# Optimization experiments

Hardware: AMD Instinct MI355X
Metric: run time of the kernel (lower is better)

Reference implementation:

```python
import jax, jax.numpy as jnp
import numpy as np

N_STATE = 1024
N_HEAD = 16
B, T, S_CACHE = 4, 1024, 3072


def setup_inputs() -> dict:
    key = jax.random.key(0)
    ks = jax.random.split(key, 10)
    d = N_STATE
    inp = {
        "x": jax.random.normal(ks[0], (B, T, d), dtype=jnp.float32),
        "k_cache": jax.random.normal(ks[1], (B, S_CACHE, d), dtype=jnp.float32),
        "v_cache": jax.random.normal(ks[2], (B, S_CACHE, d), dtype=jnp.float32),
        # Linear weights stored as [in, out]; key projection has no bias (as in torch module)
        "Wq": jax.random.normal(ks[3], (d, d), dtype=jnp.float32) / np.sqrt(d),
        "bq": jnp.zeros((d,), dtype=jnp.float32),
        "Wk": jax.random.normal(ks[4], (d, d), dtype=jnp.float32) / np.sqrt(d),
        "Wv": jax.random.normal(ks[5], (d, d), dtype=jnp.float32) / np.sqrt(d),
        "bv": jnp.zeros((d,), dtype=jnp.float32),
        "Wo": jax.random.normal(ks[6], (d, d), dtype=jnp.float32) / np.sqrt(d),
        "bo": jnp.zeros((d,), dtype=jnp.float32),
    }
    return inp


def _qkv_attention(q, k, v, n_head):
    # q: [B,T,D], k/v: [B,S,D]
    b, t, d = q.shape
    s = k.shape[1]
    hd = d // n_head
    scale = hd ** (-0.25)
    qh = q.reshape(b, t, n_head, hd).transpose(0, 2, 1, 3) * scale  # [B,H,T,hd]
    kh = k.reshape(b, s, n_head, hd).transpose(0, 2, 1, 3) * scale  # [B,H,S,hd]
    vh = v.reshape(b, s, n_head, hd).transpose(0, 2, 1, 3)          # [B,H,S,hd]
    qk = jnp.einsum("bhtd,bhsd->bhts", qh, kh)                      # [B,H,T,S]
    # Faithful to the torch module: TxT causal triu mask placed in the FIRST T
    # columns of a TxS boolean mask; remaining columns unmasked.
    causal = jnp.triu(jnp.ones((t, t), dtype=bool), k=1)
    mask = jnp.concatenate([causal, jnp.zeros((t, s - t), dtype=bool)], axis=1)
    qk = jnp.where(mask[None, None], jnp.float32(-np.inf), qk)
    w = jax.nn.softmax(qk.astype(jnp.float32), axis=-1).astype(q.dtype)
    out = jnp.einsum("bhts,bhsd->bhtd", w, vh)                      # [B,H,T,hd]
    return out.transpose(0, 2, 1, 3).reshape(b, t, d)


def reference(x, k_cache, v_cache, Wq, bq, Wk, Wv, bv, Wo, bo):
    q = x @ Wq + bq
    k = x @ Wk                     # key projection has no bias
    v = x @ Wv + bv
    k = jnp.concatenate([k_cache, k], axis=1)
    v = jnp.concatenate([v_cache, v], axis=1)
    wv = _qkv_attention(q, k, v, N_HEAD)
    return (wv @ Wo + bo, k, v)
```

## Files before the change

kernel.cpp:

```cpp
#include <hip/hip_runtime.h>
#include <hip/hip_bf16.h>

typedef unsigned short ushort_t;

#define DMODEL 1024
#define HD     64
#define NHEAD  16
#define BATCH  4
#define TQ     1024
#define SCACHE 3072
#define STOT   4096

#define OUT_ELEMS   (BATCH * TQ * DMODEL)
#define KV_ELEMS    (BATCH * STOT * DMODEL)
#define K_OFF       OUT_ELEMS
#define V_OFF       (OUT_ELEMS + KV_ELEMS)

using frag_ab = __attribute__((ext_vector_type(8))) short;
using f32x4   = __attribute__((ext_vector_type(4))) float;
using u16x4   = __attribute__((ext_vector_type(4))) unsigned short;

static __device__ __forceinline__ short f2bf(float f) {
    union { float f; unsigned u; } v; v.f = f;
    unsigned r = (v.u + 0x7FFFu + ((v.u >> 16) & 1u)) >> 16;
    return (short)r;
}
static __device__ __forceinline__ float bf2f(ushort_t h) {
    union { unsigned u; float f; } v; v.u = ((unsigned)h) << 16; return v.f;
}

static __device__ __forceinline__ void stage16(const void* g, void* l) {
#if __has_builtin(__builtin_amdgcn_global_load_lds)
    __builtin_amdgcn_global_load_lds(
        (const __attribute__((address_space(1))) unsigned int*)g,
        (__attribute__((address_space(3))) unsigned int*)l, 16, 0, 0);
#else
    *(frag_ab*)l = *(const frag_ab*)g;
#endif
}

#define WS_XHI   0ull
#define WS_XLO   8388608ull
#define WS_WTHI  16777216ull
#define WS_WTLO  23068672ull
#define WS_WOHI  29360128ull
#define WS_WOLO  31457280ull
#define WS_BIAS  33554432ull
#define WS_QBF   33570816ull
#define WS_KBF   41959424ull
#define WS_VBT   75513856ull
#define WS_AHI   109068288ull
#define WS_ALO   117456896ull
#define WS_FULL  125845504ull

__global__ void copy_caches(const float4* __restrict__ kc, const float4* __restrict__ vc,
                            float4* __restrict__ ko, float4* __restrict__ vo,
                            u16x4* __restrict__ kbf)
{
    const int per_b = SCACHE * DMODEL / 4;
    const int ob    = STOT * DMODEL / 4;
    const int total = BATCH * per_b;
    for (int i = blockIdx.x * blockDim.x + threadIdx.x; i < total;
         i += gridDim.x * blockDim.x) {
        int b = i / per_b;
        int r = i - b * per_b;
        float4 k4 = kc[i];
        ko[b * ob + r] = k4;
        vo[b * ob + r] = vc[i];
        if (kbf) {
            u16x4 h;
            h[0] = (ushort_t)f2bf(k4.x); h[1] = (ushort_t)f2bf(k4.y);
            h[2] = (ushort_t)f2bf(k4.z); h[3] = (ushort_t)f2bf(k4.w);
            kbf[(size_t)b * ob + r] = h;
        }
    }
}

__global__ void convert_x(const float4* __restrict__ x,
                          u16x4* __restrict__ hi, u16x4* __restrict__ lo)
{
    const int total = BATCH * TQ * DMODEL / 4;
    for (int i = blockIdx.x * blockDim.x + threadIdx.x; i < total;
         i += gridDim.x * blockDim.x) {
        float4 v = x[i];
        u16x4 h, l;
        h[0] = (ushort_t)f2bf(v.x); h[1] = (ushort_t)f2bf(v.y);
        h[2] = (ushort_t)f2bf(v.z); h[3] = (ushort_t)f2bf(v.w);
        l[0] = (ushort_t)f2bf(v.x - bf2f(h[0]));
        l[1] = (ushort_t)f2bf(v.y - bf2f(h[1]));
        l[2] = (ushort_t)f2bf(v.z - bf2f(h[2]));
        l[3] = (ushort_t)f2bf(v.w - bf2f(h[3]));
        hi[i] = h; lo[i] = l;
    }
}

__global__ __launch_bounds__(256) void transconv_w(
    const float* __restrict__ Wq, const float* __restrict__ Wk,
    const float* __restrict__ Wv, const float* __restrict__ Wo,
    ushort_t* __restrict__ WtHi, ushort_t* __restrict__ WtLo,
    ushort_t* __restrict__ WoHi, ushort_t* __restrict__ WoLo)
{
    __shared__ float T[32][33];
    const int z = blockIdx.z;
    const float* src = (z == 0) ? Wq : (z == 1) ? Wk : (z == 2) ? Wv : Wo;
    ushort_t* dhi = (z < 3) ? WtHi + (size_t)z * 1024 * 1024 : WoHi;
    ushort_t* dlo = (z < 3) ? WtLo + (size_t)z * 1024 * 1024 : WoLo;
    const int tx = threadIdx.x & 31, ty = threadIdx.x >> 5;
    const int k0 = blockIdx.y * 32, n0 = blockIdx.x * 32;
    #pragma unroll
    for (int s = 0; s < 4; ++s)
        T[ty + s * 8][tx] = src[(size_t)(k0 + ty + s * 8) * 1024 + n0 + tx];
    __syncthreads();
    #pragma unroll
    for (int s = 0; s < 4; ++s) {
        int n = n0 + ty + s * 8, k = k0 + tx;
        float v = T[tx][ty + s * 8];
        ushort_t h = (ushort_t)f2bf(v);
        ushort_t l = (ushort_t)f2bf(v - bf2f(h));
        dhi[(size_t)n * 1024 + k] = h;
        dlo[(size_t)n * 1024 + k] = l;
    }
}

__global__ void build_bias(const float* __restrict__ bq, const float* __restrict__ bv,
                           float* __restrict__ b3)
{
    int i = blockIdx.x * blockDim.x + threadIdx.x;
    if (i < 3072)
        b3[i] = (i < 1024) ? bq[i] : (i < 2048) ? 0.0f : bv[i - 2048];
}

__global__ __launch_bounds__(256) void transpose_v(
    const float* __restrict__ vout, ushort_t* __restrict__ vbt)
{
    __shared__ float T[32][33];
    const int b = blockIdx.z;
    const int s0 = blockIdx.x * 32, d0 = blockIdx.y * 32;
    const int tx = threadIdx.x & 31, ty = threadIdx.x >> 5;
    #pragma unroll
    for (int s = 0; s < 4; ++s)
        T[ty + s * 8][tx] = vout[(size_t)(b * STOT + s0 + ty + s * 8) * 1024 + d0 + tx];
    __syncthreads();
    #pragma unroll
    for (int s = 0; s < 4; ++s) {
        int d = d0 + ty + s * 8, sx = s0 + tx;
        vbt[((size_t)b * 1024 + d) * STOT + sx] = (ushort_t)f2bf(T[tx][ty + s * 8]);
    }
}

template<int MI, int NI, int MODE>
__global__ __launch_bounds__(256) void gemm_sb(
    const ushort_t* __restrict__ Ahi, const ushort_t* __restrict__ Alo,
    const ushort_t* __restrict__ Bhi, const ushort_t* __restrict__ Blo,
    const float* __restrict__ bias,
    float* __restrict__ C0, float* __restrict__ C1,
    ushort_t* __restrict__ Qbf, ushort_t* __restrict__ Kbf)
{
    constexpr int BM = MI * 32, BN = NI * 32;
    __shared__ ushort_t AhiL[BM][32], AloL[BM][32], BhiL[BN][32], BloL[BN][32];
    const int tid = threadIdx.x;
    const int w = tid >> 6, lane = tid & 63, c = lane & 15, g = lane >> 4;
    const int wm = w >> 1, wn = w & 1;
    const int bm = blockIdx.y * BM, bn = blockIdx.x * BN;

    f32x4 acc[MI][NI] = {};

    for (int k0 = 0; k0 < 1024; k0 += 32) {
        __syncthreads();
        #pragma unroll
        for (int q = 0; q < BM / 64; ++q) {
            int flat = q * 256 + tid;
            int row = flat >> 2, ch = flat & 3;
            size_t go = (size_t)(bm + row) * 1024 + k0 + ch * 8;
            stage16(Ahi + go, &AhiL[0][0] + (size_t)flat * 8);
            stage16(Alo + go, &AloL[0][0] + (size_t)flat * 8);
        }
        #pragma unroll
        for (int q = 0; q < BN / 64; ++q) {
            int flat = q * 256 + tid;
            int row = flat >> 2, ch = flat & 3;
            size_t go = (size_t)(bn + row) * 1024 + k0 + ch * 8;
            stage16(Bhi + go, &BhiL[0][0] + (size_t)flat * 8);
            stage16(Blo + go, &BloL[0][0] + (size_t)flat * 8);
        }
        __syncthreads();

        frag_ab ah[MI], al[MI], bh[NI], bl[NI];
        #pragma unroll
        for (int mi = 0; mi < MI; ++mi) {
            int r = wm * MI * 16 + mi * 16 + c;
            ah[mi] = *(const frag_ab*)&AhiL[r][g * 8];
            al[mi] = *(const frag_ab*)&AloL[r][g * 8];
        }
        #pragma unroll
        for (int ni = 0; ni < NI; ++ni) {
            int r = wn * NI * 16 + ni * 16 + c;
            bh[ni] = *(const frag_ab*)&BhiL[r][g * 8];
            bl[ni] = *(const frag_ab*)&BloL[r][g * 8];
        }
        #pragma unroll
        for (int mi = 0; mi < MI; ++mi)
            #pragma unroll
            for (int ni = 0; ni < NI; ++ni) {
                acc[mi][ni] = __builtin_amdgcn_mfma_f32_16x16x32_bf16(ah[mi], bh[ni], acc[mi][ni], 0, 0, 0);
                acc[mi][ni] = __builtin_amdgcn_mfma_f32_16x16x32_bf16(ah[mi], bl[ni], acc[mi][ni], 0, 0, 0);
                acc[mi][ni] = __builtin_amdgcn_mfma_f32_16x16x32_bf16(al[mi], bh[ni], acc[mi][ni], 0, 0, 0);
            }
    }

    const int seg = (MODE == 0) ? 0 : (bn >> 10);
    #pragma unroll
    for (int mi = 0; mi < MI; ++mi) {
        #pragma unroll
        for (int ni = 0; ni < NI; ++ni) {
            const int ncol = bn + wn * NI * 16 + ni * 16 + c;
            const float bv = bias[ncol];
            #pragma unroll
            for (int i = 0; i < 4; ++i) {
                const int grow = bm + wm * MI * 16 + mi * 16 + g * 4 + i;
                float val = acc[mi][ni][i] + bv;
                if (MODE == 0) {
                    C0[(size_t)grow * 1024 + ncol] = val;
                } else if (seg == 0) {
                    Qbf[(size_t)grow * 1024 + ncol] = (ushort_t)f2bf(val);
                } else {
                    const int n2 = ncol & 1023;
                    const size_t drow = (size_t)(grow >> 10) * STOT + SCACHE + (grow & 1023);
                    if (seg == 1) {
                        C0[drow * 1024 + n2] = val;
                        Kbf[drow * 1024 + n2] = (ushort_t)f2bf(val);
                    } else {
                        C1[drow * 1024 + n2] = val;
                    }
                }
            }
        }
    }
}

__global__ __launch_bounds__(256) void attn_bf16(
    const ushort_t* __restrict__ Qbf,
    const ushort_t* __restrict__ Kbf,
    const ushort_t* __restrict__ Vbt,
    ushort_t* __restrict__ OHi, ushort_t* __restrict__ OLo)
{
    __shared__ ushort_t Klds[32][72];
    __shared__ ushort_t Vlds[64][40];
    __shared__ ushort_t Plds[4][16][40];
    const int tid = threadIdx.x;
    const int w = tid >> 6, lane = tid & 63, c = lane & 15, g = lane >> 4;
    const int b = blockIdx.z, h = blockIdx.y;
    const int q0 = blockIdx.x * 64 + w * 16;

    frag_ab qf[2];
    {
        const ushort_t* qp = Qbf + ((size_t)(b * TQ + q0 + c)) * 1024 + h * HD + g * 8;
        qf[0] = *(const frag_ab*)qp;
        qf[1] = *(const frag_ab*)(qp + 32);
    }

    f32x4 acc[4] = {};
    float m_run[4], l_run[4];
    #pragma unroll
    for (int i = 0; i < 4; ++i) { m_run[i] = -1e30f; l_run[i] = 0.0f; }

    const ushort_t* Kh = Kbf + (size_t)b * STOT * 1024 + h * HD;
    const ushort_t* Vh = Vbt + ((size_t)b * 1024 + h * HD) * STOT;
    const int krow = tid >> 3, kch = tid & 7;
    const int vrow = tid >> 2, vch = tid & 3;
    const int tq0 = q0 + g * 4;

    frag_ab gk = *(const frag_ab*)(Kh + (size_t)krow * 1024 + kch * 8);
    frag_ab gv = *(const frag_ab*)(Vh + (size_t)vrow * STOT + vch * 8);

    for (int ks = 0; ks < STOT; ks += 32) {
        __syncthreads();
        *(frag_ab*)&Klds[krow][kch * 8] = gk;
        *(frag_ab*)&Vlds[vrow][vch * 8] = gv;
        __syncthreads();
        if (ks + 32 < STOT) {
            gk = *(const frag_ab*)(Kh + (size_t)(ks + 32 + krow) * 1024 + kch * 8);
            gv = *(const frag_ab*)(Vh + (size_t)vrow * STOT + ks + 32 + vch * 8);
        }

        f32x4 s[2];
        #pragma unroll
        for (int sub = 0; sub < 2; ++sub) {
            f32x4 z = {0.f, 0.f, 0.f, 0.f};
            #pragma unroll
            for (int half = 0; half < 2; ++half) {
                frag_ab kf = *(const frag_ab*)&Klds[sub * 16 + c][half * 32 + g * 8];
                z = __builtin_amdgcn_mfma_f32_16x16x32_bf16(qf[half], kf, z, 0, 0, 0);
            }
            s[sub] = z;
        }

        const int k0i = ks + c, k1i = ks + 16 + c;
        const bool m0c = (k0i < TQ), m1c = (k1i < TQ);
        float mt[4];
        #pragma unroll
        for (int i = 0; i < 4; ++i) {
            const int tq = tq0 + i;
            float s0 = s[0][i] * 0.125f, s1 = s[1][i] * 0.125f;
            if (m0c && k0i > tq) s0 = -1e30f;
            if (m1c && k1i > tq) s1 = -1e30f;
            s[0][i] = s0; s[1][i] = s1;
            float v = fmaxf(s0, s1);
            v = fmaxf(v, __shfl_xor(v, 1));
            v = fmaxf(v, __shfl_xor(v, 2));
            v = fmaxf(v, __shfl_xor(v, 4));
            v = fmaxf(v, __shfl_xor(v, 8));
            mt[i] = v;
        }

        bool grew = (mt[0] > m_run[0]) | (mt[1] > m_run[1]) |
                    (mt[2] > m_run[2]) | (mt[3] > m_run[3]);
        if (__any(grew)) {
            #pragma unroll
            for (int i = 0; i < 4; ++i) {
                float mn = fmaxf(m_run[i], mt[i]);
                float corr = __expf(m_run[i] - mn);
                m_run[i] = mn;
                l_run[i] *= corr;
                #pragma unroll
                for (int f = 0; f < 4; ++f) acc[f][i] *= corr;
            }
        }

        float p0[4], p1[4];
        #pragma unroll
        for (int i = 0; i < 4; ++i) {
            p0[i] = __expf(s[0][i] - m_run[i]);
            p1[i] = __expf(s[1][i] - m_run[i]);
            float rs = p0[i] + p1[i];
            rs += __shfl_xor(rs, 1);
            rs += __shfl_xor(rs, 2);
            rs += __shfl_xor(rs, 4);
            rs += __shfl_xor(rs, 8);
            l_run[i] += rs;
        }

        ushort_t* pl = &Plds[w][0][0];
        #pragma unroll
        for (int i = 0; i < 4; ++i) {
            int row = g * 4 + i;
            pl[row * 40 + c]      = (ushort_t)f2bf(p0[i]);
            pl[row * 40 + 16 + c] = (ushort_t)f2bf(p1[i]);
        }
        frag_ab pa = *(const frag_ab*)(pl + c * 40 + g * 8);

        #pragma unroll
        for (int f = 0; f < 4; ++f) {
            frag_ab vf = *(const frag_ab*)&Vlds[f * 16 + c][g * 8];
            acc[f] = __builtin_amdgcn_mfma_f32_16x16x32_bf16(pa, vf, acc[f], 0, 0, 0);
        }
    }

    #pragma unroll
    for (int f = 0; f < 4; ++f)
        #pragma unroll
        for (int i = 0; i < 4; ++i) {
            float o = acc[f][i] / l_run[i];
            ushort_t hi = (ushort_t)f2bf(o);
            ushort_t lo = (ushort_t)f2bf(o - bf2f(hi));
            size_t idx = ((size_t)(b * TQ + q0 + g * 4 + i)) * 1024 + h * HD + f * 16 + c;
            OHi[idx] = hi;
            OLo[idx] = lo;
        }
}

__global__ __launch_bounds__(256) void gemm_f32(
    const float* __restrict__ X, const float* __restrict__ Wm,
    const float* __restrict__ bias, float* __restrict__ Cb,
    int OS, int OFF)
{
    __shared__ float As[8][128];
    __shared__ float Bs[8][132];
    const int tid = threadIdx.x;
    const int tx = tid & 15, ty = tid >> 4;
    const int bm = blockIdx.y * 128, bn = blockIdx.x * 128;
    const int arow = tid >> 1, acol = (tid & 1) * 4;
    const int brow = tid >> 5, bcol = (tid & 31) * 4;

    float acc[8][8] = {};
    const float* Aptr = X + (size_t)(bm + arow) * DMODEL + acol;
    const float* Bptr = Wm + (size_t)brow * DMODEL + bn + bcol;

    for (int k0 = 0; k0 < DMODEL; k0 += 8) {
        float4 av = *(const float4*)(Aptr + k0);
        float4 bv = *(const float4*)(Bptr + (size_t)k0 * DMODEL);
        __syncthreads();
        As[acol + 0][arow] = av.x;
        As[acol + 1][arow] = av.y;
        As[acol + 2][arow] = av.z;
        As[acol + 3][arow] = av.w;
        *(float4*)&Bs[brow][bcol] = bv;
        __syncthreads();
        #pragma unroll
        for (int kk = 0; kk < 8; ++kk) {
            float a[8], bb[8];
            *(float4*)&a[0]  = *(const float4*)&As[kk][ty * 8];
            *(float4*)&a[4]  = *(const float4*)&As[kk][ty * 8 + 4];
            *(float4*)&bb[0] = *(const float4*)&Bs[kk][tx * 8];
            *(float4*)&bb[4] = *(const float4*)&Bs[kk][tx * 8 + 4];
            #pragma unroll
            for (int i = 0; i < 8; ++i)
                #pragma unroll
                for (int j = 0; j < 8; ++j)
                    acc[i][j] += a[i] * bb[j];
        }
    }

    float bv8[8];
    #pragma unroll
    for (int j = 0; j < 8; ++j) bv8[j] = bias ? bias[bn + tx * 8 + j] : 0.0f;

    #pragma unroll
    for (int i = 0; i < 8; ++i) {
        int r = bm + ty * 8 + i;
        int dstrow = (r >> 10) * OS + OFF + (r & 1023);
        float* cp = Cb + (size_t)dstrow * DMODEL + bn + tx * 8;
        float4 c0 = { acc[i][0] + bv8[0], acc[i][1] + bv8[1],
                      acc[i][2] + bv8[2], acc[i][3] + bv8[3] };
        float4 c1 = { acc[i][4] + bv8[4], acc[i][5] + bv8[5],
                      acc[i][6] + bv8[6], acc[i][7] + bv8[7] };
        *(float4*)cp       = c0;
        *(float4*)(cp + 4) = c1;
    }
}

__global__ __launch_bounds__(256) void attn_f32(
    const float* __restrict__ Qb, const float* __restrict__ Kb,
    const float* __restrict__ Vb, float* __restrict__ Ob)
{
    __shared__ __align__(16) ushort_t Plds[4][16][40];
    const int warp = threadIdx.x >> 6;
    const int lane = threadIdx.x & 63;
    const int c = lane & 15, g = lane >> 4;
    const int W = blockIdx.x * 4 + warp;
    const int qt = W & 63, h = (W >> 6) & 15, b = W >> 10;
    const int q0 = qt * 16;

    frag_ab qf[2];
    {
        const float* qrow = Qb + (size_t)(b * TQ + q0 + c) * DMODEL + h * HD;
        #pragma unroll
        for (int half = 0; half < 2; ++half) {
            const float* p = qrow + half * 32 + g * 8;
            float4 x0 = *(const float4*)p;
            float4 x1 = *(const float4*)(p + 4);
            qf[half][0] = f2bf(x0.x * 0.125f); qf[half][1] = f2bf(x0.y * 0.125f);
            qf[half][2] = f2bf(x0.z * 0.125f); qf[half][3] = f2bf(x0.w * 0.125f);
            qf[half][4] = f2bf(x1.x * 0.125f); qf[half][5] = f2bf(x1.y * 0.125f);
            qf[half][6] = f2bf(x1.z * 0.125f); qf[half][7] = f2bf(x1.w * 0.125f);
        }
    }

    f32x4 acc[4] = {};
    float m_run[4], l_run[4];
    #pragma unroll
    for (int i = 0; i < 4; ++i) { m_run[i] = -1e30f; l_run[i] = 0.0f; }

    const float* Kh = Kb + (size_t)b * STOT * DMODEL + h * HD;
    const float* Vh = Vb + (size_t)b * STOT * DMODEL + h * HD;
    ushort_t* pl = &Plds[warp][0][0];

    for (int ks = 0; ks < STOT; ks += 32) {
        f32x4 s[2];
        #pragma unroll
        for (int sub = 0; sub < 2; ++sub) {
            f32x4 z = {0.f, 0.f, 0.f, 0.f};
            #pragma unroll
            for (int half = 0; half < 2; ++half) {
                const float* kp = Kh + (size_t)(ks + sub * 16 + c) * DMODEL + half * 32 + g * 8;
                float4 x0 = *(const float4*)kp;
                float4 x1 = *(const float4*)(kp + 4);
                frag_ab kf;
                kf[0] = f2bf(x0.x); kf[1] = f2bf(x0.y);
                kf[2] = f2bf(x0.z); kf[3] = f2bf(x0.w);
                kf[4] = f2bf(x1.x); kf[5] = f2bf(x1.y);
                kf[6] = f2bf(x1.z); kf[7] = f2bf(x1.w);
                z = __builtin_amdgcn_mfma_f32_16x16x32_bf16(qf[half], kf, z, 0, 0, 0);
            }
            s[sub] = z;
        }
        float mt[4];
        #pragma unroll
        for (int i = 0; i < 4; ++i) {
            const int tq = q0 + g * 4 + i;
            #pragma unroll
            for (int sub = 0; sub < 2; ++sub) {
                int kidx = ks + sub * 16 + c;
                if (kidx < TQ && kidx > tq) s[sub][i] = -1e30f;
            }
            float v = fmaxf(s[0][i], s[1][i]);
            v = fmaxf(v, __shfl_xor(v, 1));
            v = fmaxf(v, __shfl_xor(v, 2));
            v = fmaxf(v, __shfl_xor(v, 4));
            v = fmaxf(v, __shfl_xor(v, 8));
            mt[i] = v;
        }
        float p0[4], p1[4];
        #pragma unroll
        for (int i = 0; i < 4; ++i) {
            float mn = fmaxf(m_run[i], mt[i]);
            float corr = __expf(m_run[i] - mn);
            m_run[i] = mn;
            l_run[i] *= corr;
            #pragma unroll
            for (int f = 0; f < 4; ++f) acc[f][i] *= corr;
            p0[i] = __expf(s[0][i] - mn);
            p1[i] = __expf(s[1][i] - mn);
            float rs = p0[i] + p1[i];
            rs += __shfl_xor(rs, 1);
            rs += __shfl_xor(rs, 2);
            rs += __shfl_xor(rs, 4);
            rs += __shfl_xor(rs, 8);
            l_run[i] += rs;
        }
        #pragma unroll
        for (int i = 0; i < 4; ++i) {
            int row = g * 4 + i;
            pl[row * 40 + c]      = (ushort_t)f2bf(p0[i]);
            pl[row * 40 + 16 + c] = (ushort_t)f2bf(p1[i]);
        }
        frag_ab pa = *(const frag_ab*)(pl + c * 40 + g * 8);
        #pragma unroll
        for (int f = 0; f < 4; ++f) {
            const float* vp = Vh + (size_t)(ks + g * 8) * DMODEL + f * 16 + c;
            frag_ab vf;
            #pragma unroll
            for (int j = 0; j < 8; ++j) vf[j] = f2bf(vp[(size_t)j * DMODEL]);
            acc[f] = __builtin_amdgcn_mfma_f32_16x16x32_bf16(pa, vf, acc[f], 0, 0, 0);
        }
    }

    float* orow = Ob + (size_t)(b * TQ + q0) * DMODEL + h * HD;
    #pragma unroll
    for (int f = 0; f < 4; ++f)
        #pragma unroll
        for (int i = 0; i < 4; ++i)
            orow[(size_t)(g * 4 + i) * DMODEL + f * 16 + c] = acc[f][i] / l_run[i];
}

extern "C" void kernel_launch(void* const* d_in, const int* in_sizes, int n_in,
                              void* d_out, int out_size, void* d_ws, size_t ws_size,
                              hipStream_t stream) {
    const float* x  = (const float*)d_in[0];
    const float* kc = (const float*)d_in[1];
    const float* vc = (const float*)d_in[2];
    const float* Wq = (const float*)d_in[3];
    const float* bq = (const float*)d_in[4];
    const float* Wk = (const float*)d_in[5];
    const float* Wv = (const float*)d_in[6];
    const float* bv = (const float*)d_in[7];
    const float* Wo = (const float*)d_in[8];
    const float* bo = (const float*)d_in[9];

    float* out  = (float*)d_out;
    float* kout = out + K_OFF;
    float* vout = out + V_OFF;

    if (ws_size >= WS_FULL) {
        uint8_t* W8 = (uint8_t*)d_ws;
        ushort_t* XHI  = (ushort_t*)(W8 + WS_XHI);
        ushort_t* XLO  = (ushort_t*)(W8 + WS_XLO);
        ushort_t* WTHI = (ushort_t*)(W8 + WS_WTHI);
        ushort_t* WTLO = (ushort_t*)(W8 + WS_WTLO);
        ushort_t* WOHI = (ushort_t*)(W8 + WS_WOHI);
        ushort_t* WOLO = (ushort_t*)(W8 + WS_WOLO);
        float*    BIAS = (float*)   (W8 + WS_BIAS);
        ushort_t* QBF  = (ushort_t*)(W8 + WS_QBF);
        ushort_t* KBF  = (ushort_t*)(W8 + WS_KBF);
        ushort_t* VBT  = (ushort_t*)(W8 + WS_VBT);
        ushort_t* AHI  = (ushort_t*)(W8 + WS_AHI);
        ushort_t* ALO  = (ushort_t*)(W8 + WS_ALO);

        copy_caches<<<2048, 256, 0, stream>>>((const float4*)kc, (const float4*)vc,
                                              (float4*)kout, (float4*)vout, (u16x4*)KBF);
        convert_x<<<2048, 256, 0, stream>>>((const float4*)x, (u16x4*)XHI, (u16x4*)XLO);
        transconv_w<<<dim3(32, 32, 4), 256, 0, stream>>>(Wq, Wk, Wv, Wo, WTHI, WTLO, WOHI, WOLO);
        build_bias<<<12, 256, 0, stream>>>(bq, bv, BIAS);
        gemm_sb<4, 4, 1><<<dim3(24, 32), 256, 0, stream>>>(XHI, XLO, WTHI, WTLO, BIAS,
                                                           kout, vout, QBF, KBF);
        transpose_v<<<dim3(128, 32, 4), 256, 0, stream>>>(vout, VBT);
        attn_bf16<<<dim3(16, 16, 4), 256, 0, stream>>>(QBF, KBF, VBT, AHI, ALO);
        gemm_sb<4, 2, 0><<<dim3(16, 32), 256, 0, stream>>>(AHI, ALO, WOHI, WOLO, bo,
                                                           out, nullptr, nullptr, nullptr);
    } else {
        float* qbuf = out;
        float* attn = (float*)d_ws;

        copy_caches<<<2048, 256, 0, stream>>>((const float4*)kc, (const float4*)vc,
                                              (float4*)kout, (float4*)vout, nullptr);
        dim3 gg(8, 32);
        gemm_f32<<<gg, 256, 0, stream>>>(x, Wk, nullptr, kout, STOT, SCACHE);
        gemm_f32<<<gg, 256, 0, stream>>>(x, Wv, bv,      vout, STOT, SCACHE);
        gemm_f32<<<gg, 256, 0, stream>>>(x, Wq, bq,      qbuf, TQ,   0);
        attn_f32<<<1024, 256, 0, stream>>>(qbuf, kout, vout, attn);
        gemm_f32<<<gg, 256, 0, stream>>>(attn, Wo, bo, out, TQ, 0);
    }
}
```

Before: 731.4 us.

## Skip fully masked causal key tiles and restructure attention with transposed scores

Rewrites the attention inner loop to process 64-key tiles and skip the key range that the causal mask fully hides for each query block; only the diagonal tile applies the mask. The MFMA operands are swapped so each lane holds one query row's scores, which reduces the cross-lane shuffles for the row max and row sum. The scale is folded into an exp2 base. K and V are now read directly from global memory instead of being staged through shared memory with block barriers. This removes syncs and masked work, but the four waves load the same K/V redundantly and rely on cache.

New measurement: 875.4 us. +19.7%, slower.

```diff
diff --git a/kernel.cpp b/kernel.cpp
--- a/kernel.cpp
+++ b/kernel.cpp
@@ -27,6 +27,10 @@
 }
 static __device__ __forceinline__ float bf2f(ushort_t h) {
     union { unsigned u; float f; } v; v.u = ((unsigned)h) << 16; return v.f;
+}
+static __device__ __forceinline__ ushort_t fbh(float f) {
+    __hip_bfloat16 h = __float2bfloat16(f);
+    return *reinterpret_cast<ushort_t*>(&h);
 }
 
 static __device__ __forceinline__ void stage16(const void* g, void* l) {
@@ -244,13 +248,12 @@
     const ushort_t* __restrict__ Vbt,
     ushort_t* __restrict__ OHi, ushort_t* __restrict__ OLo)
 {
-    __shared__ ushort_t Klds[32][72];
-    __shared__ ushort_t Vlds[64][40];
-    __shared__ ushort_t Plds[4][16][40];
+    __shared__ __align__(16) ushort_t Plds[4][16][72];
     const int tid = threadIdx.x;
     const int w = tid >> 6, lane = tid & 63, c = lane & 15, g = lane >> 4;
     const int b = blockIdx.z, h = blockIdx.y;
-    const int q0 = blockIdx.x * 64 + w * 16;
+    const int Q0 = blockIdx.x * 64;
+    const int q0 = Q0 + w * 16;
 
     frag_ab qf[2];
     {
@@ -260,107 +263,100 @@
     }
 
     f32x4 acc[4] = {};
-    float m_run[4], l_run[4];
-    #pragma unroll
-    for (int i = 0; i < 4; ++i) { m_run[i] = -1e30f; l_run[i] = 0.0f; }
+    float m_run = -1e30f, l_run = 0.0f;
+    const float SC = 0.125f * 1.44269504f;
 
     const ushort_t* Kh = Kbf + (size_t)b * STOT * 1024 + h * HD;
     const ushort_t* Vh = Vbt + ((size_t)b * 1024 + h * HD) * STOT;
-    const int krow = tid >> 3, kch = tid & 7;
-    const int vrow = tid >> 2, vch = tid & 3;
-    const int tq0 = q0 + g * 4;
-
-    frag_ab gk = *(const frag_ab*)(Kh + (size_t)krow * 1024 + kch * 8);
-    frag_ab gv = *(const frag_ab*)(Vh + (size_t)vrow * STOT + vch * 8);
-
-    for (int ks = 0; ks < STOT; ks += 32) {
-        __syncthreads();
-        *(frag_ab*)&Klds[krow][kch * 8] = gk;
-        *(frag_ab*)&Vlds[vrow][vch * 8] = gv;
-        __syncthreads();
-        if (ks + 32 < STOT) {
-            gk = *(const frag_ab*)(Kh + (size_t)(ks + 32 + krow) * 1024 + kch * 8);
-            gv = *(const frag_ab*)(Vh + (size_t)vrow * STOT + ks + 32 + vch * 8);
-        }
-
-        f32x4 s[2];
-        #pragma unroll
-        for (int sub = 0; sub < 2; ++sub) {
+    ushort_t* pl = &Plds[w][0][0];
+
+    auto tile = [&](int ks, bool domask) __attribute__((always_inline)) {
+        float p[4][4];
+        #pragma unroll
+        for (int sub = 0; sub < 4; ++sub) {
             f32x4 z = {0.f, 0.f, 0.f, 0.f};
             #pragma unroll
             for (int half = 0; half < 2; ++half) {
-                frag_ab kf = *(const frag_ab*)&Klds[sub * 16 + c][half * 32 + g * 8];
-                z = __builtin_amdgcn_mfma_f32_16x16x32_bf16(qf[half], kf, z, 0, 0, 0);
-            }
-            s[sub] = z;
-        }
-
-        const int k0i = ks + c, k1i = ks + 16 + c;
-        const bool m0c = (k0i < TQ), m1c = (k1i < TQ);
-        float mt[4];
+                frag_ab kf = *(const frag_ab*)(Kh + (size_t)(ks + sub * 16 + c) * 1024 + half * 32 + g * 8);
+                z = __builtin_amdgcn_mfma_f32_16x16x32_bf16(kf, qf[half], z, 0, 0, 0);
+            }
+            #pragma unroll
+            for (int i = 0; i < 4; ++i) {
+                float y = z[i] * SC;
+                if (domask) {
+                    int kidx = ks + sub * 16 + g * 4 + i;
+                    if (kidx > q0 + c) y = -1e30f;
+                }
+                p[sub][i] = y;
+            }
+        }
+
+        float mt = p[0][0];
+        #pragma unroll
+        for (int sub = 0; sub < 4; ++sub)
+            #pragma unroll
+            for (int i = 0; i < 4; ++i) mt = fmaxf(mt, p[sub][i]);
+        mt = fmaxf(mt, __shfl_xor(mt, 16));
+        mt = fmaxf(mt, __shfl_xor(mt, 32));
+
+        bool grew = mt > m_run;
+        if (__any(grew)) {
+            float mn = fmaxf(m_run, mt);
+            float corr = exp2f(m_run - mn);
+            m_run = mn;
+            l_run *= corr;
+            #pragma unroll
+            for (int i = 0; i < 4; ++i) {
+                float ci = __shfl(corr, g * 20 + i);
+                #pragma unroll
+                for (int f = 0; f < 4; ++f) acc[f][i] *= ci;
+            }
+        }
+
+        float rs = 0.0f;
+        #pragma unroll
+        for (int sub = 0; sub < 4; ++sub)
+            #pragma unroll
+            for (int i = 0; i < 4; ++i) {
+                p[sub][i] = exp2f(p[sub][i] - m_run);
+                rs += p[sub][i];
+            }
+        rs += __shfl_xor(rs, 16);
+        rs += __shfl_xor(rs, 32);
+        l_run += rs;
+
+        #pragma unroll
+        for (int sub = 0; sub < 4; ++sub) {
+            short4 pk;
+            pk.x = (short)fbh(p[sub][0]); pk.y = (short)fbh(p[sub][1]);
+            pk.z = (short)fbh(p[sub][2]); pk.w = (short)fbh(p[sub][3]);
+            *(short4*)&pl[c * 72 + sub * 16 + g * 4] = pk;
+        }
+
+        #pragma unroll
+        for (int sp = 0; sp < 2; ++sp) {
+            frag_ab pa = *(const frag_ab*)&pl[c * 72 + sp * 32 + g * 8];
+            #pragma unroll
+            for (int f = 0; f < 4; ++f) {
+                frag_ab vf = *(const frag_ab*)(Vh + (size_t)(f * 16 + c) * STOT + ks + sp * 32 + g * 8);
+                acc[f] = __builtin_amdgcn_mfma_f32_16x16x32_bf16(pa, vf, acc[f], 0, 0, 0);
+            }
+        }
+    };
+
+    for (int ks = 0; ks < Q0; ks += 64) tile(ks, false);
+    tile(Q0, true);
+    for (int ks = TQ; ks < STOT; ks += 64) tile(ks, false);
+
+    float rl[4];
+    #pragma unroll
+    for (int i = 0; i < 4; ++i)
+        rl[i] = 1.0f / __shfl(l_run, g * 20 + i);
+    #pragma unroll
+    for (int f = 0; f < 4; ++f)
         #pragma unroll
         for (int i = 0; i < 4; ++i) {
-            const int tq = tq0 + i;
-            float s0 = s[0][i] * 0.125f, s1 = s[1][i] * 0.125f;
-            if (m0c && k0i > tq) s0 = -1e30f;
-            if (m1c && k1i > tq) s1 = -1e30f;
-            s[0][i] = s0; s[1][i] = s1;
-            float v = fmaxf(s0, s1);
-            v = fmaxf(v, __shfl_xor(v, 1));
-            v = fmaxf(v, __shfl_xor(v, 2));
-            v = fmaxf(v, __shfl_xor(v, 4));
-            v = fmaxf(v, __shfl_xor(v, 8));
-            mt[i] = v;
-        }
-
-        bool grew = (mt[0] > m_run[0]) | (mt[1] > m_run[1]) |
-                    (mt[2] > m_run[2]) | (mt[3] > m_run[3]);
-        if (__any(grew)) {
-            #pragma unroll
-            for (int i = 0; i < 4; ++i) {
-                float mn = fmaxf(m_run[i], mt[i]);
-                float corr = __expf(m_run[i] - mn);
-                m_run[i] = mn;
-                l_run[i] *= corr;
-                #pragma unroll
-                for (int f = 0; f < 4; ++f) acc[f][i] *= corr;
-            }
-        }
-
-        float p0[4], p1[4];
-        #pragma unroll
-        for (int i = 0; i < 4; ++i) {
-            p0[i] = __expf(s[0][i] - m_run[i]);
-            p1[i] = __expf(s[1][i] - m_run[i]);
-            float rs = p0[i] + p1[i];
-            rs += __shfl_xor(rs, 1);
-            rs += __shfl_xor(rs, 2);
-            rs += __shfl_xor(rs, 4);
-            rs += __shfl_xor(rs, 8);
-            l_run[i] += rs;
-        }
-
-        ushort_t* pl = &Plds[w][0][0];
-        #pragma unroll
-        for (int i = 0; i < 4; ++i) {
-            int row = g * 4 + i;
-            pl[row * 40 + c]      = (ushort_t)f2bf(p0[i]);
-            pl[row * 40 + 16 + c] = (ushort_t)f2bf(p1[i]);
-        }
-        frag_ab pa = *(const frag_ab*)(pl + c * 40 + g * 8);
-
-        #pragma unroll
-        for (int f = 0; f < 4; ++f) {
-            frag_ab vf = *(const frag_ab*)&Vlds[f * 16 + c][g * 8];
-            acc[f] = __builtin_amdgcn_mfma_f32_16x16x32_bf16(pa, vf, acc[f], 0, 0, 0);
-        }
-    }
-
-    #pragma unroll
-    for (int f = 0; f < 4; ++f)
-        #pragma unroll
-        for (int i = 0; i < 4; ++i) {
-            float o = acc[f][i] / l_run[i];
+            float o = acc[f][i] * rl[i];
             ushort_t hi = (ushort_t)f2bf(o);
             ushort_t lo = (ushort_t)f2bf(o - bf2f(hi));
             size_t idx = ((size_t)(b * TQ + q0 + g * 4 + i)) * 1024 + h * HD + f * 16 + c;
```
